# Performance work log

Hardware: AMD Instinct MI355X
Metric: run time of the kernel (lower is better)

Reference implementation:

```python
import jax, jax.numpy as jnp
import numpy as np

N_TOKENS = 32768
D_MODEL = 1024


def setup_inputs() -> dict:
    key = jax.random.key(0)
    kx, kr, kw1, kb1, kw2, kb2 = jax.random.split(key, 6)
    scale = 1.0 / np.sqrt(D_MODEL)
    x = jax.random.normal(kx, (N_TOKENS, D_MODEL), dtype=jnp.float32)
    # RandomScatterRouter: each token independently routed to one of 2 experts
    route = jax.random.randint(kr, (N_TOKENS,), 0, 2, dtype=jnp.int32)
    W1 = jax.random.normal(kw1, (D_MODEL, D_MODEL), dtype=jnp.float32) * scale
    b1 = jax.random.normal(kb1, (D_MODEL,), dtype=jnp.float32) * scale
    W2 = jax.random.normal(kw2, (D_MODEL, D_MODEL), dtype=jnp.float32) * scale
    b2 = jax.random.normal(kb2, (D_MODEL,), dtype=jnp.float32) * scale
    return {"x": x, "W1": W1, "b1": b1, "W2": W2, "b2": b2, "route": route}


def reference(x, W1, b1, W2, b2, route):
    # Semantics of scatter -> expert linears -> gather(reverse_indice):
    #   out[i] = x[i] @ W_{route[i]} + b_{route[i]}  (original token order restored)
    # jit-friendly form: mask-partition tokens to each expert (m0 + m1 == 1),
    # run the two expert GEMMs on the disjoint partitions, sum to recombine.
    m0 = (route == 0).astype(x.dtype)[:, None]  # [N, 1]
    m1 = 1.0 - m0
    y0 = (x * m0) @ W1 + b1 * m0  # expert-1 output on its tokens, zeros elsewhere
    y1 = (x * m1) @ W2 + b2 * m1  # expert-2 output on its tokens, zeros elsewhere
    return y0 + y1
```

## Files before the change

kernel.cpp:

```cpp
#include <hip/hip_runtime.h>

#define NT 32768
#define DM 1024
#define NTOT (NT + 128)

typedef __bf16 bf16x8 __attribute__((ext_vector_type(8)));
typedef float f32x4 __attribute__((ext_vector_type(4)));

#define GLD16(g, l)                                                            \
  __builtin_amdgcn_global_load_lds(                                            \
      (const __attribute__((address_space(1))) void*)(g),                      \
      (__attribute__((address_space(3))) void*)(l), 16, 0, 0)

__device__ __forceinline__ unsigned short f2bf(float f) {
  unsigned u = __float_as_uint(f);
  u += 0x7fffu + ((u >> 16) & 1u);
  return (unsigned short)(u >> 16);
}

__global__ void wt_k(const float* __restrict__ W, unsigned short* __restrict__ Wt) {
  __shared__ float tile[32][33];
  int tx = threadIdx.x, ty = threadIdx.y;
  int n0 = blockIdx.x * 32, k0 = blockIdx.y * 32;
#pragma unroll
  for (int i = 0; i < 32; i += 8)
    tile[ty + i][tx] = W[(size_t)(k0 + ty + i) * DM + n0 + tx];
  __syncthreads();
#pragma unroll
  for (int i = 0; i < 32; i += 8)
    Wt[(size_t)(n0 + ty + i) * DM + k0 + tx] = f2bf(tile[tx][ty + i]);
}

__global__ __launch_bounds__(256) void part_k(
    const float* __restrict__ x, const int* __restrict__ route,
    unsigned short* __restrict__ xp, int* __restrict__ idx,
    int* __restrict__ counters) {
  __shared__ int slots[64];
  const int t = threadIdx.x, lane = t & 63, wave = t >> 6;
  const int tok0 = blockIdx.x * 64;

  if (wave == 0) {
    int token = tok0 + lane;
    int r = route[token];
    unsigned long long m0 = __ballot(r == 0);
    unsigned long long lt = (1ULL << lane) - 1ULL;
    int rank0 = __popcll(m0 & lt);
    int rank1 = lane - rank0;
    int cnt0 = __popcll(m0);
    int base0 = 0, base1 = 0;
    if (lane == 0) {
      base0 = atomicAdd(&counters[0], cnt0);
      base1 = atomicAdd(&counters[1], 64 - cnt0);
    }
    base0 = __shfl(base0, 0, 64);
    base1 = __shfl(base1, 0, 64);
    int slot = (r == 0) ? (base0 + rank0) : (NTOT - 1 - (base1 + rank1));
    slots[lane] = slot;
    idx[slot] = token;
  }
  __syncthreads();

  for (int row = wave; row < 64; row += 4) {
    const float4* src = (const float4*)(x + (size_t)(tok0 + row) * DM);
    unsigned short* dst = xp + (size_t)slots[row] * DM;
#pragma unroll
    for (int p = 0; p < 4; ++p) {
      float4 v = src[p * 64 + lane];
      union { unsigned short h[4]; ushort4 u4; } pk;
      pk.h[0] = f2bf(v.x); pk.h[1] = f2bf(v.y);
      pk.h[2] = f2bf(v.z); pk.h[3] = f2bf(v.w);
      *(ushort4*)(dst + (size_t)(p * 64 + lane) * 4) = pk.u4;
    }
  }
}

__global__ __launch_bounds__(256, 4) void gemm_k(
    const unsigned short* __restrict__ xp,
    const unsigned short* __restrict__ Wt,
    const float* __restrict__ b1, const float* __restrict__ b2,
    const int* __restrict__ idx, const int* __restrict__ counters,
    float* __restrict__ out) {
  __shared__ unsigned short As[128 * 64];
  __shared__ unsigned short Bs[128 * 64];

  const int t = threadIdx.x;
  const int lane = t & 63, wave = t >> 6;
  const int row0 = blockIdx.y * 128;
  const int col0 = blockIdx.x * 128;
  const int n0 = counters[0];
  const int expert = (row0 < n0) ? 0 : 1;
  const unsigned short* Wte = Wt + (size_t)expert * DM * DM;
  const float* bias = expert ? b2 : b1;

  const int wr = (wave >> 1) * 64;
  const int wc = (wave & 1) * 64;
  const int lr = lane & 15;

  f32x4 acc[4][4] = {};

  for (int k0 = 0; k0 < DM; k0 += 64) {
#pragma unroll
    for (int p = 0; p < 4; ++p) {
      int q = p * 256 + t;
      int r = q >> 3;
      int c = ((q & 7) ^ (r & 7)) * 8;
      GLD16(xp  + (size_t)(row0 + r) * DM + k0 + c, As + q * 8);
      GLD16(Wte + (size_t)(col0 + r) * DM + k0 + c, Bs + q * 8);
    }
    __syncthreads();
#pragma unroll
    for (int s = 0; s < 2; ++s) {
      const int cb = s * 4 + (lane >> 4);
      bf16x8 af[4], bfr[4];
#pragma unroll
      for (int i = 0; i < 4; ++i) {
        int r = wr + i * 16 + lr;
        af[i] = *(const bf16x8*)&As[(r * 8 + (cb ^ (r & 7))) * 8];
      }
#pragma unroll
      for (int j = 0; j < 4; ++j) {
        int r = wc + j * 16 + lr;
        bfr[j] = *(const bf16x8*)&Bs[(r * 8 + (cb ^ (r & 7))) * 8];
      }
#pragma unroll
      for (int i = 0; i < 4; ++i)
#pragma unroll
        for (int j = 0; j < 4; ++j)
          acc[i][j] = __builtin_amdgcn_mfma_f32_16x16x32_bf16(af[i], bfr[j], acc[i][j], 0, 0, 0);
    }
    __syncthreads();
  }

#pragma unroll
  for (int i = 0; i < 4; ++i) {
#pragma unroll
    for (int reg = 0; reg < 4; ++reg) {
      int gr = row0 + wr + i * 16 + (lane >> 4) * 4 + reg;
      if (gr < n0 || gr >= n0 + 128) {
        int dest = idx[gr];
#pragma unroll
        for (int j = 0; j < 4; ++j) {
          int gc = col0 + wc + j * 16 + (lane & 15);
          out[(size_t)dest * DM + gc] = acc[i][j][reg] + bias[gc];
        }
      }
    }
  }
}

extern "C" void kernel_launch(void* const* d_in, const int* in_sizes, int n_in,
                              void* d_out, int out_size, void* d_ws, size_t ws_size,
                              hipStream_t stream) {
  const float* x   = (const float*)d_in[0];
  const float* W1  = (const float*)d_in[1];
  const float* b1  = (const float*)d_in[2];
  const float* W2  = (const float*)d_in[3];
  const float* b2  = (const float*)d_in[4];
  const int*   route = (const int*)d_in[5];
  float* out = (float*)d_out;

  char* ws = (char*)d_ws;
  unsigned short* xp = (unsigned short*)ws;
  size_t off = (size_t)NTOT * DM * 2;
  unsigned short* Wt = (unsigned short*)(ws + off);
  off += (size_t)2 * DM * DM * 2;
  int* idx = (int*)(ws + off);
  int* counters = idx + NTOT;

  hipMemsetAsync(counters, 0, 2 * sizeof(int), stream);
  part_k<<<NT / 64, 256, 0, stream>>>(x, route, xp, idx, counters);
  wt_k<<<dim3(DM / 32, DM / 32), dim3(32, 8), 0, stream>>>(W1, Wt);
  wt_k<<<dim3(DM / 32, DM / 32), dim3(32, 8), 0, stream>>>(W2, Wt + (size_t)DM * DM);
  gemm_k<<<dim3(DM / 128, NTOT / 128), 256, 0, stream>>>(xp, Wt, b1, b2, idx, counters, out);
}
```

Baseline: 358.7 us.

## Fuse fp32 gather and bf16 conversion into double-buffered GEMM A-loads

Removes the separate pass that gathered x rows into a partitioned bf16 buffer. The GEMM now gathers fp32 rows through idx and converts them to bf16 in registers before writing LDS, with double-buffered A/B tiles so next-tile loads overlap the MFMAs. It also remaps blocks so the 8 column tiles of a row group are spread across the grid, merges the two weight transposes into one launch, and lowers launch_bounds occupancy to 2. The cost is reading fp32 x eight times (once per column tile) instead of bf16, plus more registers and LDS per block.

```diff
diff --git a/kernel.cpp b/kernel.cpp
--- a/kernel.cpp
+++ b/kernel.cpp
@@ -3,6 +3,7 @@
 #define NT 32768
 #define DM 1024
 #define NTOT (NT + 128)
+#define NKT (DM / 64)
 
 typedef __bf16 bf16x8 __attribute__((ext_vector_type(8)));
 typedef float f32x4 __attribute__((ext_vector_type(4)));
@@ -18,7 +19,10 @@
   return (unsigned short)(u >> 16);
 }
 
-__global__ void wt_k(const float* __restrict__ W, unsigned short* __restrict__ Wt) {
+__global__ void wt_k(const float* __restrict__ W1, const float* __restrict__ W2,
+                     unsigned short* __restrict__ Wt) {
+  const float* __restrict__ W = blockIdx.z ? W2 : W1;
+  unsigned short* __restrict__ dst = Wt + (size_t)blockIdx.z * DM * DM;
   __shared__ float tile[32][33];
   int tx = threadIdx.x, ty = threadIdx.y;
   int n0 = blockIdx.x * 32, k0 = blockIdx.y * 32;
@@ -28,65 +32,48 @@
   __syncthreads();
 #pragma unroll
   for (int i = 0; i < 32; i += 8)
-    Wt[(size_t)(n0 + ty + i) * DM + k0 + tx] = f2bf(tile[tx][ty + i]);
+    dst[(size_t)(n0 + ty + i) * DM + k0 + tx] = f2bf(tile[tx][ty + i]);
 }
 
-__global__ __launch_bounds__(256) void part_k(
-    const float* __restrict__ x, const int* __restrict__ route,
-    unsigned short* __restrict__ xp, int* __restrict__ idx,
-    int* __restrict__ counters) {
-  __shared__ int slots[64];
-  const int t = threadIdx.x, lane = t & 63, wave = t >> 6;
-  const int tok0 = blockIdx.x * 64;
-
-  if (wave == 0) {
-    int token = tok0 + lane;
-    int r = route[token];
-    unsigned long long m0 = __ballot(r == 0);
-    unsigned long long lt = (1ULL << lane) - 1ULL;
-    int rank0 = __popcll(m0 & lt);
-    int rank1 = lane - rank0;
-    int cnt0 = __popcll(m0);
-    int base0 = 0, base1 = 0;
-    if (lane == 0) {
-      base0 = atomicAdd(&counters[0], cnt0);
-      base1 = atomicAdd(&counters[1], 64 - cnt0);
-    }
-    base0 = __shfl(base0, 0, 64);
-    base1 = __shfl(base1, 0, 64);
-    int slot = (r == 0) ? (base0 + rank0) : (NTOT - 1 - (base1 + rank1));
-    slots[lane] = slot;
-    idx[slot] = token;
+__global__ __launch_bounds__(64) void route_k(const int* __restrict__ route,
+                                              int* __restrict__ idx,
+                                              int* __restrict__ counters) {
+  const int lane = threadIdx.x;
+  const int token = blockIdx.x * 64 + lane;
+  int r = route[token];
+  unsigned long long m0 = __ballot(r == 0);
+  unsigned long long lt = (1ULL << lane) - 1ULL;
+  int rank0 = __popcll(m0 & lt);
+  int rank1 = lane - rank0;
+  int cnt0 = __popcll(m0);
+  int base0 = 0, base1 = 0;
+  if (lane == 0) {
+    base0 = atomicAdd(&counters[0], cnt0);
+    base1 = atomicAdd(&counters[1], 64 - cnt0);
   }
-  __syncthreads();
-
-  for (int row = wave; row < 64; row += 4) {
-    const float4* src = (const float4*)(x + (size_t)(tok0 + row) * DM);
-    unsigned short* dst = xp + (size_t)slots[row] * DM;
-#pragma unroll
-    for (int p = 0; p < 4; ++p) {
-      float4 v = src[p * 64 + lane];
-      union { unsigned short h[4]; ushort4 u4; } pk;
-      pk.h[0] = f2bf(v.x); pk.h[1] = f2bf(v.y);
-      pk.h[2] = f2bf(v.z); pk.h[3] = f2bf(v.w);
-      *(ushort4*)(dst + (size_t)(p * 64 + lane) * 4) = pk.u4;
-    }
-  }
+  base0 = __shfl(base0, 0, 64);
+  base1 = __shfl(base1, 0, 64);
+  int slot = (r == 0) ? (base0 + rank0) : (NTOT - 1 - (base1 + rank1));
+  idx[slot] = token;
 }
 
-__global__ __launch_bounds__(256, 4) void gemm_k(
-    const unsigned short* __restrict__ xp,
+__global__ __launch_bounds__(256, 2) void gemm_k(
+    const float* __restrict__ x,
     const unsigned short* __restrict__ Wt,
     const float* __restrict__ b1, const float* __restrict__ b2,
     const int* __restrict__ idx, const int* __restrict__ counters,
     float* __restrict__ out) {
-  __shared__ unsigned short As[128 * 64];
-  __shared__ unsigned short Bs[128 * 64];
+  __shared__ unsigned short As[2][128 * 64];
+  __shared__ unsigned short Bs[2][128 * 64];
 
   const int t = threadIdx.x;
   const int lane = t & 63, wave = t >> 6;
-  const int row0 = blockIdx.y * 128;
-  const int col0 = blockIdx.x * 128;
+
+  const int lin = blockIdx.y * 8 + blockIdx.x;
+  const int L = (lin & 7) * 257 + (lin >> 3);
+  const int row0 = (L >> 3) * 128;
+  const int col0 = (L & 7) * 128;
+
   const int n0 = counters[0];
   const int expert = (row0 < n0) ? 0 : 1;
   const unsigned short* Wte = Wt + (size_t)expert * DM * DM;
@@ -96,18 +83,53 @@
   const int wc = (wave & 1) * 64;
   const int lr = lane & 15;
 
+  const int rsub = t >> 4;
+  const int c16 = t & 15;
+  const float* rowp[8];
+#pragma unroll
+  for (int p = 0; p < 8; ++p) {
+    int gr = row0 + p * 16 + rsub;
+    int tok = idx[gr];
+    if (gr >= n0 && gr < n0 + 128) tok = 0;
+    rowp[p] = x + (size_t)tok * DM;
+  }
+
+  float4 a[8];
   f32x4 acc[4][4] = {};
 
-  for (int k0 = 0; k0 < DM; k0 += 64) {
-#pragma unroll
-    for (int p = 0; p < 4; ++p) {
-      int q = p * 256 + t;
-      int r = q >> 3;
-      int c = ((q & 7) ^ (r & 7)) * 8;
-      GLD16(xp  + (size_t)(row0 + r) * DM + k0 + c, As + q * 8);
-      GLD16(Wte + (size_t)(col0 + r) * DM + k0 + c, Bs + q * 8);
+#define LOADA(k0)                                                              \
+  _Pragma("unroll") for (int p = 0; p < 8; ++p)                                \
+      a[p] = *(const float4*)(rowp[p] + (k0) + c16 * 4);
+
+#define WRITEA(bufw)                                                           \
+  _Pragma("unroll") for (int p = 0; p < 8; ++p) {                              \
+    int r = p * 16 + rsub;                                                     \
+    int off = (r * 8 + ((c16 >> 1) ^ (r & 7))) * 16 + (c16 & 1) * 8;           \
+    union { unsigned short h[4]; ushort4 u4; } pk;                             \
+    pk.h[0] = f2bf(a[p].x); pk.h[1] = f2bf(a[p].y);                            \
+    pk.h[2] = f2bf(a[p].z); pk.h[3] = f2bf(a[p].w);                            \
+    *(ushort4*)((char*)&As[bufw][0] + off) = pk.u4;                            \
+  }
+
+#define STAGEB(k0, bufw)                                                       \
+  _Pragma("unroll") for (int p = 0; p < 4; ++p) {                              \
+    int q = p * 256 + t;                                                       \
+    int r = q >> 3;                                                            \
+    int c = ((q & 7) ^ (r & 7)) * 8;                                           \
+    GLD16(Wte + (size_t)(col0 + r) * DM + (k0) + c, &Bs[bufw][q * 8]);         \
+  }
+
+  LOADA(0);
+  STAGEB(0, 0);
+  WRITEA(0);
+  __syncthreads();
+
+  for (int kt = 0; kt < NKT; ++kt) {
+    const int buf = kt & 1;
+    if (kt < NKT - 1) {
+      LOADA((kt + 1) * 64);
+      STAGEB((kt + 1) * 64, buf ^ 1);
     }
-    __syncthreads();
 #pragma unroll
     for (int s = 0; s < 2; ++s) {
       const int cb = s * 4 + (lane >> 4);
@@ -115,12 +137,12 @@
 #pragma unroll
       for (int i = 0; i < 4; ++i) {
         int r = wr + i * 16 + lr;
-        af[i] = *(const bf16x8*)&As[(r * 8 + (cb ^ (r & 7))) * 8];
+        af[i] = *(const bf16x8*)&As[buf][(r * 8 + (cb ^ (r & 7))) * 8];
       }
 #pragma unroll
       for (int j = 0; j < 4; ++j) {
         int r = wc + j * 16 + lr;
-        bfr[j] = *(const bf16x8*)&Bs[(r * 8 + (cb ^ (r & 7))) * 8];
+        bfr[j] = *(const bf16x8*)&Bs[buf][(r * 8 + (cb ^ (r & 7))) * 8];
       }
 #pragma unroll
       for (int i = 0; i < 4; ++i)
@@ -128,6 +150,7 @@
         for (int j = 0; j < 4; ++j)
           acc[i][j] = __builtin_amdgcn_mfma_f32_16x16x32_bf16(af[i], bfr[j], acc[i][j], 0, 0, 0);
     }
+    if (kt < NKT - 1) WRITEA(buf ^ 1);
     __syncthreads();
   }
 
@@ -146,6 +169,9 @@
       }
     }
   }
+#undef LOADA
+#undef WRITEA
+#undef STAGEB
 }
 
 extern "C" void kernel_launch(void* const* d_in, const int* in_sizes, int n_in,
@@ -160,16 +186,13 @@
   float* out = (float*)d_out;
 
   char* ws = (char*)d_ws;
-  unsigned short* xp = (unsigned short*)ws;
-  size_t off = (size_t)NTOT * DM * 2;
-  unsigned short* Wt = (unsigned short*)(ws + off);
-  off += (size_t)2 * DM * DM * 2;
+  unsigned short* Wt = (unsigned short*)ws;
+  size_t off = (size_t)2 * DM * DM * 2;
   int* idx = (int*)(ws + off);
   int* counters = idx + NTOT;
 
   hipMemsetAsync(counters, 0, 2 * sizeof(int), stream);
-  part_k<<<NT / 64, 256, 0, stream>>>(x, route, xp, idx, counters);
-  wt_k<<<dim3(DM / 32, DM / 32), dim3(32, 8), 0, stream>>>(W1, Wt);
-  wt_k<<<dim3(DM / 32, DM / 32), dim3(32, 8), 0, stream>>>(W2, Wt + (size_t)DM * DM);
-  gemm_k<<<dim3(DM / 128, NTOT / 128), 256, 0, stream>>>(xp, Wt, b1, b2, idx, counters, out);
+  route_k<<<NT / 64, 64, 0, stream>>>(route, idx, counters);
+  wt_k<<<dim3(DM / 32, DM / 32, 2), dim3(32, 8), 0, stream>>>(W1, W2, Wt);
+  gemm_k<<<dim3(8, NTOT / 128), 256, 0, stream>>>(x, Wt, b1, b2, idx, counters, out);
 }
```

Result: slower. 417.0 us (+16.3%).
